# Kernel optimization log

Measured on AMD Instinct MI355X. Metric: run time of the kernel, lower is better.

The kernel has to match this reference:

```python
import jax, jax.numpy as jnp
import numpy as np

N = 20000      # nodes (all graphs in batch)
E = 320000     # edges (avg degree 16)
G = 16         # graphs in batch
D_IN = 32      # raw node feature dim
D_LAP = 16     # laplacian PE dim
D = 256        # d_model
H = 8          # heads
DH = D // H    # head dim
L = 2          # encoder layers
D_FF = 2 * D   # FFN hidden (FFN_layer1: d_model -> 2*d_model)
EPS = 1e-5


def _layer_norm(x, g, b):
    m = jnp.mean(x, axis=-1, keepdims=True)
    v = jnp.var(x, axis=-1, keepdims=True)
    return g * (x - m) * jax.lax.rsqrt(v + EPS) + b


def setup_inputs() -> dict:
    key = jax.random.key(0)
    ks = jax.random.split(key, 32)

    feat = jax.random.normal(ks[0], (N, D_IN), dtype=jnp.float32)
    lap_pos = jax.random.normal(ks[1], (N, D_LAP), dtype=jnp.float32)
    # random +-1 sign flip per PE dim (done with torch.rand in the original forward)
    sign_flip = jnp.where(jax.random.uniform(ks[2], (D_LAP,)) >= 0.5, 1.0, -1.0).astype(jnp.float32)

    src = jax.random.randint(ks[3], (E,), 0, N, dtype=jnp.int32)
    dst = jax.random.randint(ks[4], (E,), 0, N, dtype=jnp.int32)
    graph_ids = jnp.sort(jax.random.randint(ks[5], (N,), 0, G, dtype=jnp.int32))

    def xavier(k, shape):
        fan_in, fan_out = shape[-2], shape[-1]
        lim = np.sqrt(6.0 / (fan_in + fan_out))
        return jax.random.uniform(k, shape, minval=-lim, maxval=lim, dtype=jnp.float32)

    inp = {
        "feat": feat, "lap_pos": lap_pos, "sign_flip": sign_flip,
        "src": src, "dst": dst, "graph_ids": graph_ids,
        # input embeddings
        "Wh": xavier(ks[6], (D_IN, D)), "bh": jnp.zeros((D,), jnp.float32),
        "Wlp": xavier(ks[7], (D_LAP, D)), "blp": jnp.zeros((D,), jnp.float32),
        # per-layer params, stacked on leading layer axis
        "Wq": xavier(ks[8], (L, D, D)), "Wk": xavier(ks[9], (L, D, D)),
        "Wv": xavier(ks[10], (L, D, D)),
        "Wo": xavier(ks[11], (L, D, D)), "bo": jnp.zeros((L, D), jnp.float32),
        "g1": jnp.ones((L, D), jnp.float32), "b1": jnp.zeros((L, D), jnp.float32),
        "W1": xavier(ks[12], (L, D, D_FF)), "c1": jnp.zeros((L, D_FF), jnp.float32),
        "W2": xavier(ks[13], (L, D_FF, D)), "c2": jnp.zeros((L, D), jnp.float32),
        "g2": jnp.ones((L, D), jnp.float32), "b2": jnp.zeros((L, D), jnp.float32),
    }
    return inp


def _forward(feat, lap_pos, sign_flip, src, dst, graph_ids,
             Wh, bh, Wlp, blp, Wq, Wk, Wv, Wo, bo, g1, b1, W1, c1, W2, c2, g2, b2):
    scale = np.sqrt(DH).astype(np.float32)

    h = feat @ Wh + bh                                  # [N, D]
    h = h + (lap_pos * sign_flip[None, :]) @ Wlp + blp  # add PE embedding

    for l in range(L):
        h_in1 = h
        Q = (h @ Wq[l]).reshape(N, H, DH)
        K = (h @ Wk[l]).reshape(N, H, DH)
        V = (h @ Wv[l]).reshape(N, H, DH)

        # per-edge dot-product score, then exp(clamp(score/sqrt(dh), -5, 5))
        score = jnp.sum(K[src] * Q[dst], axis=-1)                       # [E, H]
        s = jnp.exp(jnp.clip(score / scale, -5.0, 5.0))                # [E, H]

        # segment softmax of s over incoming edges per dst node (F.softmax on mailbox)
        m = jax.ops.segment_max(s, dst, num_segments=N)                 # [N, H], -inf if no in-edges
        p = jnp.exp(s - m[dst])                                         # [E, H]
        den = jax.ops.segment_sum(p, dst, num_segments=N)               # [N, H]
        msg = jax.ops.segment_sum(p[:, :, None] * V[src], dst, num_segments=N)  # [N, H, DH]
        attn = msg / jnp.where(den > 0, den, 1.0)[:, :, None]
        attn = attn.reshape(N, D)

        h = _layer_norm(h_in1 + attn @ Wo[l] + bo[l], g1[l], b1[l])
        h_in2 = h
        ff = jax.nn.relu(h @ W1[l] + c1[l]) @ W2[l] + c2[l]
        h = _layer_norm(h_in2 + ff, g2[l], b2[l])

    # mean readout per graph
    counts = jax.ops.segment_sum(jnp.ones((N,), h.dtype), graph_ids, num_segments=G)
    sums = jax.ops.segment_sum(h, graph_ids, num_segments=G)            # [G, D]
    return sums / jnp.where(counts > 0, counts, 1.0)[:, None]


def reference(feat, lap_pos, sign_flip, src, dst, graph_ids,
              Wh, bh, Wlp, blp, Wq, Wk, Wv, Wo, bo, g1, b1, W1, c1, W2, c2, g2, b2):
    return _forward(feat, lap_pos, sign_flip, src, dst, graph_ids,
                    Wh, bh, Wlp, blp, Wq, Wk, Wv, Wo, bo, g1, b1, W1, c1, W2, c2, g2, b2)
```

## Files before the change

### kernel.cpp

```cpp
#include <hip/hip_runtime.h>
#include <hip/hip_bf16.h>

#define NN   20000
#define EE   320000
#define GG   16
#define DD   256
#define HH   8
#define DHH  32
#define LLAYERS 2
#define DFF  512
#define DIN  32
#define DLAP 16
#define RSPLITS 16

typedef __attribute__((ext_vector_type(8))) short bf16x8;
typedef __attribute__((ext_vector_type(8))) unsigned short u16x8;
typedef __attribute__((ext_vector_type(4))) float f32x4;

__device__ __forceinline__ void gld_lds16(const void* g, void* l) {
  __builtin_amdgcn_global_load_lds((const __attribute__((address_space(1))) uint32_t*)g,
                                   (__attribute__((address_space(3))) uint32_t*)l, 16, 0, 0);
}

__device__ __forceinline__ float b2f(unsigned short s) {
  union { unsigned int i; float f; } u;
  u.i = ((unsigned int)s) << 16;
  return u.f;
}

__device__ __forceinline__ unsigned short f2bu(float f) {
  __hip_bfloat16 b = __float2bfloat16(f);
  return *(unsigned short*)&b;
}

__global__ __launch_bounds__(256) void k_embed(
    const float* __restrict__ feat, const float* __restrict__ lap,
    const float* __restrict__ sign, const float* __restrict__ Wh,
    const float* __restrict__ bh, const float* __restrict__ Wlp,
    const float* __restrict__ blp, float* __restrict__ h,
    __hip_bfloat16* __restrict__ hb) {
  int d = threadIdx.x;
  const float bias = bh[d] + blp[d];
  for (int n = blockIdx.x; n < NN; n += gridDim.x) {
    float acc = bias;
    const float* frow = feat + (size_t)n * DIN;
    const float* lrow = lap + (size_t)n * DLAP;
#pragma unroll
    for (int k = 0; k < DIN; ++k) acc += frow[k] * Wh[k * DD + d];
#pragma unroll
    for (int k = 0; k < DLAP; ++k) acc += (lrow[k] * sign[k]) * Wlp[k * DD + d];
    h[(size_t)n * DD + d] = acc;
    hb[(size_t)n * DD + d] = __float2bfloat16(acc);
  }
}

__global__ __launch_bounds__(256) void k_wt_all(
    const float* __restrict__ Wq, const float* __restrict__ Wk,
    const float* __restrict__ Wv, const float* __restrict__ Wo,
    const float* __restrict__ W1, const float* __restrict__ W2,
    __hip_bfloat16* __restrict__ Wqt, __hip_bfloat16* __restrict__ Wkt,
    __hip_bfloat16* __restrict__ Wvt, __hip_bfloat16* __restrict__ Wot,
    __hip_bfloat16* __restrict__ W1t, __hip_bfloat16* __restrict__ W2t) {
  __shared__ float tile[32][33];
  int z = blockIdx.z;
  const float* in;
  __hip_bfloat16* out;
  int K, N, l;
  if (z < 8) {
    int widx = z >> 1;
    l = z & 1;
    K = DD; N = DD;
    in = (widx == 0) ? Wq : (widx == 1) ? Wk : (widx == 2) ? Wv : Wo;
    out = (widx == 0) ? Wqt : (widx == 1) ? Wkt : (widx == 2) ? Wvt : Wot;
  } else if (z < 10) {
    l = z - 8; K = DD; N = DFF; in = W1; out = W1t;
  } else {
    l = z - 10; K = DFF; N = DD; in = W2; out = W2t;
  }
  int bx = blockIdx.x, by = blockIdx.y;
  if (bx * 32 >= N || by * 32 >= K) return;
  const float* inl = in + (size_t)l * K * N;
  __hip_bfloat16* outl = out + (size_t)l * N * K;
  int tx = threadIdx.x & 31, ty = threadIdx.x >> 5;
#pragma unroll
  for (int i = 0; i < 32; i += 8)
    tile[ty + i][tx] = inl[(size_t)(by * 32 + ty + i) * N + bx * 32 + tx];
  __syncthreads();
#pragma unroll
  for (int i = 0; i < 32; i += 8)
    outl[(size_t)(bx * 32 + ty + i) * K + by * 32 + tx] = __float2bfloat16(tile[tx][ty + i]);
}

template <int BM, bool BIAS, bool RELU, bool KVPACK, bool OUTF32>
__global__ __launch_bounds__(256) void gemm_mfma(
    const __hip_bfloat16* __restrict__ A,
    const __hip_bfloat16* __restrict__ Bt0, const __hip_bfloat16* __restrict__ Bt1,
    const __hip_bfloat16* __restrict__ Bt2,
    const float* __restrict__ bias,
    void* __restrict__ C0, void* __restrict__ C1,
    int M, int K, int ldc0) {
  const __hip_bfloat16* Bt = (blockIdx.z == 0) ? Bt0 : (blockIdx.z == 1) ? Bt1 : Bt2;
  void* Cout = (blockIdx.z == 0) ? C0 : C1;
  const int vo = (blockIdx.z == 2) ? 4 : 0;

  constexpr int RI = BM / 32;
  __shared__ short lA[2][4][BM][8];
  __shared__ short lB[2][4][128][8];

  const int t = threadIdx.x;
  const int lane = t & 63, w = t >> 6;
  const int bm = blockIdx.x * BM, bn = blockIdx.y * 128;
  const int wrow = (w >> 1) * (BM / 2), wc = w & 1;
  const int fr = lane & 15, fg = lane >> 4;

  f32x4 acc[RI][4] = {};

  auto stage = [&](int buf, int kt) {
    const int k0 = kt * 32;
#pragma unroll
    for (int it = 0; it < BM / 64; ++it) {
      const int cbase = it * 256 + w * 64;
      const int c = cbase + lane;
      const int g = c / BM, r = c % BM;
      int arow = bm + r;
      if (arow >= M) arow = M - 1;
      gld_lds16(A + (size_t)arow * K + k0 + g * 8,
                (short*)lA + ((size_t)buf * (4 * BM) + cbase) * 8);
    }
#pragma unroll
    for (int it = 0; it < 2; ++it) {
      const int cbase = it * 256 + w * 64;
      const int c = cbase + lane;
      const int g = c >> 7, r = c & 127;
      gld_lds16(Bt + (size_t)(bn + r) * K + k0 + g * 8,
                (short*)lB + ((size_t)buf * 512 + cbase) * 8);
    }
  };

  const int nt = K >> 5;
  stage(0, 0);
  for (int kt = 0; kt < nt; ++kt) {
    const int buf = kt & 1;
    __syncthreads();
    if (kt + 1 < nt) stage(buf ^ 1, kt + 1);
    bf16x8 af[RI], bfr[4];
#pragma unroll
    for (int i = 0; i < RI; ++i)
      af[i] = *(const bf16x8*)&lA[buf][fg][wrow + i * 16 + fr][0];
#pragma unroll
    for (int j = 0; j < 4; ++j)
      bfr[j] = *(const bf16x8*)&lB[buf][fg][wc * 64 + j * 16 + fr][0];
#pragma unroll
    for (int i = 0; i < RI; ++i)
#pragma unroll
      for (int j = 0; j < 4; ++j)
        acc[i][j] = __builtin_amdgcn_mfma_f32_16x16x32_bf16(af[i], bfr[j], acc[i][j], 0, 0, 0);
  }

#pragma unroll
  for (int i = 0; i < RI; ++i) {
    const int row0 = bm + wrow + i * 16 + fg * 4;
#pragma unroll
    for (int j = 0; j < 4; ++j) {
      const int col = bn + wc * 64 + j * 16 + fr;
      float bv = BIAS ? bias[col] : 0.f;
#pragma unroll
      for (int r = 0; r < 4; ++r) {
        const int row = row0 + r;
        if (row >= M) continue;
        float v = acc[i][j][r] + bv;
        if (RELU) v = fmaxf(v, 0.f);
        if (KVPACK && blockIdx.z != 0) {
          ((__hip_bfloat16*)Cout)[(size_t)row * (2 * DD) + ((col >> 2) << 3) + vo + (col & 3)] =
              __float2bfloat16(v);
        } else if (OUTF32) {
          ((float*)Cout)[(size_t)row * ldc0 + col] = v;
        } else {
          ((__hip_bfloat16*)Cout)[(size_t)row * ldc0 + col] = __float2bfloat16(v);
        }
      }
    }
  }
}

__global__ __launch_bounds__(256) void k_ln(
    float* __restrict__ h, const float* __restrict__ add,
    const float* __restrict__ g, const float* __restrict__ b,
    __hip_bfloat16* __restrict__ hb, int n) {
  int row = blockIdx.x * 4 + (threadIdx.x >> 6);
  int lane = threadIdx.x & 63;
  if (row >= n) return;
  const size_t base = (size_t)row * DD;
  float x[4];
  float s = 0.f;
#pragma unroll
  for (int j = 0; j < 4; ++j) {
    int d = lane + j * 64;
    x[j] = h[base + d] + add[base + d];
    s += x[j];
  }
#pragma unroll
  for (int o = 32; o > 0; o >>= 1) s += __shfl_xor(s, o, 64);
  float mean = s * (1.f / 256.f);
  float vs = 0.f;
#pragma unroll
  for (int j = 0; j < 4; ++j) {
    float d = x[j] - mean;
    vs += d * d;
  }
#pragma unroll
  for (int o = 32; o > 0; o >>= 1) vs += __shfl_xor(vs, o, 64);
  float rs = rsqrtf(vs * (1.f / 256.f) + 1e-5f);
#pragma unroll
  for (int j = 0; j < 4; ++j) {
    int d = lane + j * 64;
    float v = g[d] * ((x[j] - mean) * rs) + b[d];
    h[base + d] = v;
    hb[base + d] = __float2bfloat16(v);
  }
}

__global__ void k_hist(const int* __restrict__ dst, int* __restrict__ deg, int n) {
  int i = blockIdx.x * blockDim.x + threadIdx.x;
  if (i < n) atomicAdd(&deg[dst[i]], 1);
}

__global__ __launch_bounds__(256) void k_scan_block(
    const int* __restrict__ in, int* __restrict__ ex, int* __restrict__ bsum, int n) {
  __shared__ int sm[256];
  int t = threadIdx.x;
  int i = blockIdx.x * 256 + t;
  int v = (i < n) ? in[i] : 0;
  sm[t] = v;
  __syncthreads();
  for (int o = 1; o < 256; o <<= 1) {
    int x = (t >= o) ? sm[t - o] : 0;
    __syncthreads();
    sm[t] += x;
    __syncthreads();
  }
  if (i < n) ex[i] = sm[t] - v;
  if (t == 255) bsum[blockIdx.x] = sm[255];
}

__global__ void k_finish_indptr(const int* __restrict__ ex, const int* __restrict__ bsum,
                                int* __restrict__ indptr, int* __restrict__ cursor,
                                int n, int total) {
  int i = blockIdx.x * 256 + threadIdx.x;
  if (i < n) {
    int blk = i >> 8;
    int off = 0;
    for (int x = 0; x < blk; ++x) off += bsum[x];
    int v = ex[i] + off;
    indptr[i] = v;
    cursor[i] = v;
  }
  if (i == 0) indptr[n] = total;
}

__global__ void k_fill(const int* __restrict__ dst, const int* __restrict__ src,
                       int* __restrict__ cursor, int* __restrict__ csr_src, int n) {
  int i = blockIdx.x * blockDim.x + threadIdx.x;
  if (i < n) {
    int pos = atomicAdd(&cursor[dst[i]], 1);
    csr_src[pos] = src[i];
  }
}

__global__ void k_bounds(const int* __restrict__ gid, int* __restrict__ gb, int n) {
  int i = blockIdx.x * blockDim.x + threadIdx.x;
  if (i >= n) return;
  int g = gid[i];
  if (i == 0) {
    for (int x = 0; x <= g; ++x) gb[x] = 0;
  } else {
    int pg = gid[i - 1];
    for (int x = pg + 1; x <= g; ++x) gb[x] = i;
  }
  if (i == n - 1) {
    for (int x = g + 1; x <= GG; ++x) gb[x] = n;
  }
}

__global__ __launch_bounds__(256) void k_attn(
    const int* __restrict__ indptr, const int* __restrict__ csr_src,
    const __hip_bfloat16* __restrict__ Q, const __hip_bfloat16* __restrict__ kvb,
    __hip_bfloat16* __restrict__ attn) {
  const int wid0 = blockIdx.x * 4 + (threadIdx.x >> 6);
  const int NW = gridDim.x * 4;
  const int lane = threadIdx.x & 63;
  const int half = lane >> 5;
  const int sl = lane & 31;
  const int doff = sl * 8;
  const unsigned short* kvp = (const unsigned short*)kvb;

  for (int n = wid0; n < NN; n += NW) {
    int s0 = indptr[n], s1 = indptr[n + 1];
    unsigned short* outp = (unsigned short*)attn + (size_t)n * DD + doff;

    u16x8 qv = *(const u16x8*)((const unsigned short*)Q + (size_t)n * DD + doff);
    float q[8];
#pragma unroll
    for (int i = 0; i < 8; ++i) q[i] = b2f((unsigned short)qv[i]);

    float m = 0.f, den = 0.f;
    float a[8] = {};

    int j = s0 + half;
    if (j < s1) {
      const unsigned short* row = kvp + (size_t)csr_src[j] * (2 * DD) + sl * 16;
      u16x8 c0 = *(const u16x8*)row;
      u16x8 c1 = *(const u16x8*)(row + 8);
      for (; j < s1; j += 2) {
        int jn = (j + 2 < s1) ? j + 2 : j;
        const unsigned short* rown = kvp + (size_t)csr_src[jn] * (2 * DD) + sl * 16;
        u16x8 n0 = *(const u16x8*)rown;
        u16x8 n1 = *(const u16x8*)(rown + 8);

        float dot = q[0] * b2f((unsigned short)c0[0]) + q[1] * b2f((unsigned short)c0[1]) +
                    q[2] * b2f((unsigned short)c0[2]) + q[3] * b2f((unsigned short)c0[3]) +
                    q[4] * b2f((unsigned short)c1[0]) + q[5] * b2f((unsigned short)c1[1]) +
                    q[6] * b2f((unsigned short)c1[2]) + q[7] * b2f((unsigned short)c1[3]);
        dot += __shfl_xor(dot, 1);
        dot += __shfl_xor(dot, 2);
        float x = fminf(fmaxf(dot * 0.17677669529663687f, -5.f), 5.f);
        float s = __expf(x);
        if (s - m > 8.f) {
          float r = __expf(m - s);
          den *= r;
#pragma unroll
          for (int i = 0; i < 8; ++i) a[i] *= r;
          m = s;
        }
        float p = __expf(s - m);
        den += p;
        a[0] += p * b2f((unsigned short)c0[4]);
        a[1] += p * b2f((unsigned short)c0[5]);
        a[2] += p * b2f((unsigned short)c0[6]);
        a[3] += p * b2f((unsigned short)c0[7]);
        a[4] += p * b2f((unsigned short)c1[4]);
        a[5] += p * b2f((unsigned short)c1[5]);
        a[6] += p * b2f((unsigned short)c1[6]);
        a[7] += p * b2f((unsigned short)c1[7]);
        c0 = n0;
        c1 = n1;
      }
    }

    float mo = __shfl_xor(m, 32);
    float M = fmaxf(m, mo);
    float r = __expf(m - M);
    den *= r;
#pragma unroll
    for (int i = 0; i < 8; ++i) a[i] *= r;
    den += __shfl_xor(den, 32);
#pragma unroll
    for (int i = 0; i < 8; ++i) a[i] += __shfl_xor(a[i], 32);

    if (half == 0) {
      float inv = 1.f / (den > 0.f ? den : 1.f);
      u16x8 o;
#pragma unroll
      for (int i = 0; i < 8; ++i) o[i] = f2bu(a[i] * inv);
      *(u16x8*)outp = o;
    }
  }
}

__global__ __launch_bounds__(256) void k_gmean(
    const float* __restrict__ h, const int* __restrict__ gb,
    float* __restrict__ gsum) {
  int g = blockIdx.x, s = blockIdx.y;
  int t = threadIdx.x;
  int r0 = gb[g], r1 = gb[g + 1];
  int len = r1 - r0;
  int per = (len + RSPLITS - 1) / RSPLITS;
  int a = r0 + s * per;
  int b = min(r1, a + per);
  if (a >= b) return;
  float acc = 0.f;
  for (int r = a; r < b; ++r) acc += h[(size_t)r * DD + t];
  atomicAdd(&gsum[g * DD + t], acc);
}

__global__ void k_final(const float* __restrict__ gsum, const int* __restrict__ gb,
                        float* __restrict__ out) {
  int g = blockIdx.x, t = threadIdx.x;
  int len = gb[g + 1] - gb[g];
  out[g * DD + t] = gsum[g * DD + t] / (len > 0 ? (float)len : 1.f);
}

extern "C" void kernel_launch(void* const* d_in, const int* in_sizes, int n_in,
                              void* d_out, int out_size, void* d_ws, size_t ws_size,
                              hipStream_t stream) {
  const float* feat = (const float*)d_in[0];
  const float* lap  = (const float*)d_in[1];
  const float* sign = (const float*)d_in[2];
  const int* srcs   = (const int*)d_in[3];
  const int* dsts   = (const int*)d_in[4];
  const int* gids   = (const int*)d_in[5];
  const float* Wh   = (const float*)d_in[6];
  const float* bh   = (const float*)d_in[7];
  const float* Wlp  = (const float*)d_in[8];
  const float* blp  = (const float*)d_in[9];
  const float* Wq   = (const float*)d_in[10];
  const float* Wk   = (const float*)d_in[11];
  const float* Wv   = (const float*)d_in[12];
  const float* Wo   = (const float*)d_in[13];
  const float* bo   = (const float*)d_in[14];
  const float* g1   = (const float*)d_in[15];
  const float* b1   = (const float*)d_in[16];
  const float* W1   = (const float*)d_in[17];
  const float* c1   = (const float*)d_in[18];
  const float* W2   = (const float*)d_in[19];
  const float* c2   = (const float*)d_in[20];
  const float* g2   = (const float*)d_in[21];
  const float* b2   = (const float*)d_in[22];

  char* base = (char*)d_ws;
  size_t off = 0;
  auto take = [&](size_t bytes) -> void* {
    void* p = base + off;
    off += (bytes + 255) & ~(size_t)255;
    return p;
  };
  float* h      = (float*)take((size_t)NN * DD * 4);
  float* tmp    = (float*)take((size_t)NN * DD * 4);
  __hip_bfloat16* hb  = (__hip_bfloat16*)take((size_t)NN * DD * 2);
  __hip_bfloat16* Qb  = (__hip_bfloat16*)take((size_t)NN * DD * 2);
  __hip_bfloat16* kvb = (__hip_bfloat16*)take((size_t)NN * 2 * DD * 2);
  __hip_bfloat16* t1b = (__hip_bfloat16*)take((size_t)NN * DFF * 2);
  __hip_bfloat16* Wqt = (__hip_bfloat16*)take((size_t)LLAYERS * DD * DD * 2);
  __hip_bfloat16* Wkt = (__hip_bfloat16*)take((size_t)LLAYERS * DD * DD * 2);
  __hip_bfloat16* Wvt = (__hip_bfloat16*)take((size_t)LLAYERS * DD * DD * 2);
  __hip_bfloat16* Wot = (__hip_bfloat16*)take((size_t)LLAYERS * DD * DD * 2);
  __hip_bfloat16* W1t = (__hip_bfloat16*)take((size_t)LLAYERS * DD * DFF * 2);
  __hip_bfloat16* W2t = (__hip_bfloat16*)take((size_t)LLAYERS * DFF * DD * 2);
  int* deg     = (int*)take((size_t)NN * 4);
  int* ex      = (int*)take((size_t)NN * 4);
  int* bsum    = (int*)take(256 * 4);
  int* indptr  = (int*)take((size_t)(NN + 1) * 4);
  int* cursor  = (int*)take((size_t)NN * 4);
  int* csr_src = (int*)take((size_t)EE * 4);
  int* gb      = (int*)take((size_t)(GG + 1) * 4);
  float* gsum  = (float*)take((size_t)GG * DD * 4);
  __hip_bfloat16* attnb = Qb;

  const int NB = (NN + 255) / 256;

  k_wt_all<<<dim3(DFF / 32, DFF / 32, 12), 256, 0, stream>>>(
      Wq, Wk, Wv, Wo, W1, W2, Wqt, Wkt, Wvt, Wot, W1t, W2t);

  hipMemsetAsync(deg, 0, (size_t)NN * 4, stream);
  k_hist<<<(EE + 255) / 256, 256, 0, stream>>>(dsts, deg, EE);
  k_scan_block<<<NB, 256, 0, stream>>>(deg, ex, bsum, NN);
  k_finish_indptr<<<NB, 256, 0, stream>>>(ex, bsum, indptr, cursor, NN, EE);
  k_fill<<<(EE + 255) / 256, 256, 0, stream>>>(dsts, srcs, cursor, csr_src, EE);
  k_bounds<<<NB, 256, 0, stream>>>(gids, gb, NN);

  k_embed<<<2048, 256, 0, stream>>>(feat, lap, sign, Wh, bh, Wlp, blp, h, hb);

  const int MB128 = (NN + 127) / 128;
  const int MB64  = (NN + 63) / 64;
  dim3 gQKV(MB128, DD / 128, 3);
  dim3 gD64(MB64, DD / 128, 1);
  dim3 gF64(MB64, DFF / 128, 1);

  for (int l = 0; l < LLAYERS; ++l) {
    const __hip_bfloat16* Wqt_l = Wqt + (size_t)l * DD * DD;
    const __hip_bfloat16* Wkt_l = Wkt + (size_t)l * DD * DD;
    const __hip_bfloat16* Wvt_l = Wvt + (size_t)l * DD * DD;
    const __hip_bfloat16* Wot_l = Wot + (size_t)l * DD * DD;
    const __hip_bfloat16* W1t_l = W1t + (size_t)l * DD * DFF;
    const __hip_bfloat16* W2t_l = W2t + (size_t)l * DFF * DD;
    const float* bo_l = bo + (size_t)l * DD;
    const float* g1_l = g1 + (size_t)l * DD;
    const float* b1_l = b1 + (size_t)l * DD;
    const float* c1_l = c1 + (size_t)l * DFF;
    const float* c2_l = c2 + (size_t)l * DD;
    const float* g2_l = g2 + (size_t)l * DD;
    const float* b2_l = b2 + (size_t)l * DD;

    gemm_mfma<128, false, false, true, false><<<gQKV, 256, 0, stream>>>(
        hb, Wqt_l, Wkt_l, Wvt_l, nullptr, Qb, kvb, NN, DD, DD);

    k_attn<<<2048, 256, 0, stream>>>(indptr, csr_src, Qb, kvb, attnb);

    gemm_mfma<64, true, false, false, true><<<gD64, 256, 0, stream>>>(
        attnb, Wot_l, Wot_l, Wot_l, bo_l, tmp, tmp, NN, DD, DD);
    k_ln<<<NN / 4, 256, 0, stream>>>(h, tmp, g1_l, b1_l, hb, NN);

    gemm_mfma<64, true, true, false, false><<<gF64, 256, 0, stream>>>(
        hb, W1t_l, W1t_l, W1t_l, c1_l, t1b, t1b, NN, DD, DFF);
    gemm_mfma<64, true, false, false, true><<<gD64, 256, 0, stream>>>(
        t1b, W2t_l, W2t_l, W2t_l, c2_l, tmp, tmp, NN, DFF, DD);
    k_ln<<<NN / 4, 256, 0, stream>>>(h, tmp, g2_l, b2_l, hb, NN);
  }

  hipMemsetAsync(gsum, 0, (size_t)GG * DD * 4, stream);
  k_gmean<<<dim3(GG, RSPLITS), 256, 0, stream>>>(h, gb, gsum);
  k_final<<<GG, 256, 0, stream>>>(gsum, gb, (float*)d_out);
}
```

Measured before the change: 432.8 us.

## Store GEMM residual outputs in bf16, fuse graph bounds, shrink QKV tile

The Wo and FFN2 GEMMs now write their output in bf16 rather than fp32, and the layernorm kernel reads that bf16 tensor, which halves the traffic for the intermediate. The graph-boundary computation is folded into the indptr finishing kernel, removing one launch. The QKV GEMM moves from 128-row to 64-row tiles, giving more blocks. The bf16 intermediate adds rounding error to the residual add before layernorm.

```diff
diff --git a/kernel.cpp b/kernel.cpp
--- a/kernel.cpp
+++ b/kernel.cpp
@@ -184,19 +184,20 @@
 }
 
 __global__ __launch_bounds__(256) void k_ln(
-    float* __restrict__ h, const float* __restrict__ add,
+    float* __restrict__ h, const __hip_bfloat16* __restrict__ add,
     const float* __restrict__ g, const float* __restrict__ b,
     __hip_bfloat16* __restrict__ hb, int n) {
   int row = blockIdx.x * 4 + (threadIdx.x >> 6);
   int lane = threadIdx.x & 63;
   if (row >= n) return;
   const size_t base = (size_t)row * DD;
+  const unsigned short* addp = (const unsigned short*)add + base;
   float x[4];
   float s = 0.f;
 #pragma unroll
   for (int j = 0; j < 4; ++j) {
     int d = lane + j * 64;
-    x[j] = h[base + d] + add[base + d];
+    x[j] = h[base + d] + b2f(addp[d]);
     s += x[j];
   }
 #pragma unroll
@@ -245,6 +246,7 @@
 
 __global__ void k_finish_indptr(const int* __restrict__ ex, const int* __restrict__ bsum,
                                 int* __restrict__ indptr, int* __restrict__ cursor,
+                                const int* __restrict__ gid, int* __restrict__ gb,
                                 int n, int total) {
   int i = blockIdx.x * 256 + threadIdx.x;
   if (i < n) {
@@ -254,6 +256,16 @@
     int v = ex[i] + off;
     indptr[i] = v;
     cursor[i] = v;
+    int g = gid[i];
+    if (i == 0) {
+      for (int x = 0; x <= g; ++x) gb[x] = 0;
+    } else {
+      int pg = gid[i - 1];
+      for (int x = pg + 1; x <= g; ++x) gb[x] = i;
+    }
+    if (i == n - 1) {
+      for (int x = g + 1; x <= GG; ++x) gb[x] = n;
+    }
   }
   if (i == 0) indptr[n] = total;
 }
@@ -264,21 +276,6 @@
   if (i < n) {
     int pos = atomicAdd(&cursor[dst[i]], 1);
     csr_src[pos] = src[i];
-  }
-}
-
-__global__ void k_bounds(const int* __restrict__ gid, int* __restrict__ gb, int n) {
-  int i = blockIdx.x * blockDim.x + threadIdx.x;
-  if (i >= n) return;
-  int g = gid[i];
-  if (i == 0) {
-    for (int x = 0; x <= g; ++x) gb[x] = 0;
-  } else {
-    int pg = gid[i - 1];
-    for (int x = pg + 1; x <= g; ++x) gb[x] = i;
-  }
-  if (i == n - 1) {
-    for (int x = g + 1; x <= GG; ++x) gb[x] = n;
   }
 }
 
@@ -425,7 +422,7 @@
     return p;
   };
   float* h      = (float*)take((size_t)NN * DD * 4);
-  float* tmp    = (float*)take((size_t)NN * DD * 4);
+  __hip_bfloat16* tmpb = (__hip_bfloat16*)take((size_t)NN * DD * 2);
   __hip_bfloat16* hb  = (__hip_bfloat16*)take((size_t)NN * DD * 2);
   __hip_bfloat16* Qb  = (__hip_bfloat16*)take((size_t)NN * DD * 2);
   __hip_bfloat16* kvb = (__hip_bfloat16*)take((size_t)NN * 2 * DD * 2);
@@ -454,15 +451,13 @@
   hipMemsetAsync(deg, 0, (size_t)NN * 4, stream);
   k_hist<<<(EE + 255) / 256, 256, 0, stream>>>(dsts, deg, EE);
   k_scan_block<<<NB, 256, 0, stream>>>(deg, ex, bsum, NN);
-  k_finish_indptr<<<NB, 256, 0, stream>>>(ex, bsum, indptr, cursor, NN, EE);
+  k_finish_indptr<<<NB, 256, 0, stream>>>(ex, bsum, indptr, cursor, gids, gb, NN, EE);
   k_fill<<<(EE + 255) / 256, 256, 0, stream>>>(dsts, srcs, cursor, csr_src, EE);
-  k_bounds<<<NB, 256, 0, stream>>>(gids, gb, NN);
 
   k_embed<<<2048, 256, 0, stream>>>(feat, lap, sign, Wh, bh, Wlp, blp, h, hb);
 
-  const int MB128 = (NN + 127) / 128;
-  const int MB64  = (NN + 63) / 64;
-  dim3 gQKV(MB128, DD / 128, 3);
+  const int MB64 = (NN + 63) / 64;
+  dim3 gQKV(MB64, DD / 128, 3);
   dim3 gD64(MB64, DD / 128, 1);
   dim3 gF64(MB64, DFF / 128, 1);
 
@@ -481,20 +476,20 @@
     const float* g2_l = g2 + (size_t)l * DD;
     const float* b2_l = b2 + (size_t)l * DD;
 
-    gemm_mfma<128, false, false, true, false><<<gQKV, 256, 0, stream>>>(
+    gemm_mfma<64, false, false, true, false><<<gQKV, 256, 0, stream>>>(
         hb, Wqt_l, Wkt_l, Wvt_l, nullptr, Qb, kvb, NN, DD, DD);
 
     k_attn<<<2048, 256, 0, stream>>>(indptr, csr_src, Qb, kvb, attnb);
 
-    gemm_mfma<64, true, false, false, true><<<gD64, 256, 0, stream>>>(
-        attnb, Wot_l, Wot_l, Wot_l, bo_l, tmp, tmp, NN, DD, DD);
-    k_ln<<<NN / 4, 256, 0, stream>>>(h, tmp, g1_l, b1_l, hb, NN);
+    gemm_mfma<64, true, false, false, false><<<gD64, 256, 0, stream>>>(
+        attnb, Wot_l, Wot_l, Wot_l, bo_l, tmpb, tmpb, NN, DD, DD);
+    k_ln<<<NN / 4, 256, 0, stream>>>(h, tmpb, g1_l, b1_l, hb, NN);
 
     gemm_mfma<64, true, true, false, false><<<gF64, 256, 0, stream>>>(
         hb, W1t_l, W1t_l, W1t_l, c1_l, t1b, t1b, NN, DD, DFF);
-    gemm_mfma<64, true, false, false, true><<<gD64, 256, 0, stream>>>(
-        t1b, W2t_l, W2t_l, W2t_l, c2_l, tmp, tmp, NN, DFF, DD);
-    k_ln<<<NN / 4, 256, 0, stream>>>(h, tmp, g2_l, b2_l, hb, NN);
+    gemm_mfma<64, true, false, false, false><<<gD64, 256, 0, stream>>>(
+        t1b, W2t_l, W2t_l, W2t_l, c2_l, tmpb, tmpb, NN, DFF, DD);
+    k_ln<<<NN / 4, 256, 0, stream>>>(h, tmpb, g2_l, b2_l, hb, NN);
   }
 
   hipMemsetAsync(gsum, 0, (size_t)GG * DD * 4, stream);
```

Result: no change. 433.6 us (+0.2%).
